# Optimization experiments

Hardware: AMD Instinct MI355X
Metric: run time of the kernel (lower is better)

The kernel has to match this reference:

```python
import jax, jax.numpy as jnp
import numpy as np

B, C, H, W = 4, 256, 64, 64
CQ = C // 8  # query/key projection dim


def setup_inputs() -> dict:
    key = jax.random.key(0)
    ks = jax.random.split(key, 8)
    s = 0.02
    return {
        "x": jax.random.normal(ks[0], (B, C, H, W), dtype=jnp.float32),
        "Wq": jax.random.normal(ks[1], (CQ, C), dtype=jnp.float32) * s,
        "bq": jnp.zeros((CQ,), dtype=jnp.float32),
        "Wk": jax.random.normal(ks[2], (CQ, C), dtype=jnp.float32) * s,
        "bk": jnp.zeros((CQ,), dtype=jnp.float32),
        "Wv": jax.random.normal(ks[3], (C, C), dtype=jnp.float32) * s,
        "bv": jnp.zeros((C,), dtype=jnp.float32),
        "gamma": jnp.zeros((1,), dtype=jnp.float32),
    }


def reference(x, Wq, bq, Wk, bk, Wv, bv, gamma):
    b, c, h, w = x.shape
    n = h * w
    xf = x.reshape(b, c, n)  # (B, C, N)
    # 1x1 convs == channel-wise linear maps
    q = jnp.einsum('oc,bcn->bon', Wq, xf) + bq[None, :, None]  # (B, C/8, N)
    k = jnp.einsum('oc,bcn->bon', Wk, xf) + bk[None, :, None]  # (B, C/8, N)
    v = jnp.einsum('oc,bcn->bon', Wv, xf) + bv[None, :, None]  # (B, C, N)
    # energy[b, n, m] = q[b, :, n] . k[b, :, m], scaled by sqrt(C)
    energy = jnp.einsum('bon,bom->bnm', q, k) / jnp.sqrt(jnp.asarray(c, x.dtype))
    attn = jax.nn.softmax(energy, axis=-1)  # softmax over keys m
    # out[b, c, m] = sum_n v[b, c, n] * attn[b, m, n]  (torch bmm(value, attn^T))
    out = jnp.einsum('bcn,bmn->bcm', v, attn)
    out = out.reshape(b, c, h, w)
    return gamma[0] * out + x
```

## Files before the change

kernel.cpp:

```cpp
#include <hip/hip_runtime.h>
#include <stdint.h>

#define B_ 4
#define C_ 256
#define N_ 4096
#define LOG2E 1.44269504088896341f
#define EXP2(x) __builtin_amdgcn_exp2f(x)

typedef __attribute__((ext_vector_type(8))) short short8;
typedef __attribute__((ext_vector_type(4))) float f32x4;

__device__ __forceinline__ unsigned short f2bf(float f) {
    unsigned int u = __float_as_uint(f);
    u += 0x7FFFu + ((u >> 16) & 1u);
    return (unsigned short)(u >> 16);
}

__device__ __forceinline__ unsigned int pack_bf(float a, float b) {
    unsigned int ua = __float_as_uint(a) + 0x8000u;
    unsigned int ub = __float_as_uint(b) + 0x8000u;
    return __builtin_amdgcn_perm(ub, ua, 0x07060302u);
}
__device__ __forceinline__ float bf_lo(unsigned int u) { return __uint_as_float(u << 16); }
__device__ __forceinline__ float bf_hi(unsigned int u) { return __uint_as_float(u & 0xFFFF0000u); }

__global__ __launch_bounds__(64) void prep_kernel(
    const float* __restrict__ Wq, const float* __restrict__ bq,
    const float* __restrict__ Wk, const float* __restrict__ bk,
    const float* __restrict__ Wv, const float* __restrict__ bv,
    unsigned short* __restrict__ wb, float* __restrict__ bb)
{
    const int m = blockIdx.x;
    const int t = threadIdx.x;
    const float* src;
    float scale = 1.0f, bias;
    if (m < 32)      { src = Wq + m * C_;        scale = 0.0625f * LOG2E; bias = bq[m] * 0.0625f * LOG2E; }
    else if (m < 64) { src = Wk + (m - 32) * C_;                          bias = bk[m - 32]; }
    else             { src = Wv + (m - 64) * C_;                          bias = bv[m - 64]; }
    float4 v = *(const float4*)(src + t * 4);
    unsigned int lo = (unsigned int)f2bf(v.x * scale) | ((unsigned int)f2bf(v.y * scale) << 16);
    unsigned int hi = (unsigned int)f2bf(v.z * scale) | ((unsigned int)f2bf(v.w * scale) << 16);
    *(uint2*)(wb + m * C_ + t * 4) = make_uint2(lo, hi);
    if (t == 0) bb[m] = bias;
}

__global__ __launch_bounds__(256) void proj_kernel(
    const float* __restrict__ x,
    const unsigned short* __restrict__ wb, const float* __restrict__ bb,
    unsigned short* __restrict__ qT, unsigned short* __restrict__ kT,
    unsigned short* __restrict__ vfrag)
{
    __shared__ unsigned short xs[256][68];

    const int bid = ((blockIdx.x & 7) << 5) + (blockIdx.x >> 3);
    const int b = bid >> 6, n0 = (bid & 63) << 6;
    const int jt = n0 >> 6;
    const int tid = threadIdx.x, wid = tid >> 6, lane = tid & 63;
    const int l15 = lane & 15, l4 = lane >> 4;

#pragma unroll
    for (int it = 0; it < 16; ++it) {
        int idx = it * 256 + tid;
        int k = idx >> 4, n4 = (idx & 15) << 2;
        float4 v = *(const float4*)(x + ((size_t)(b * C_ + k)) * N_ + n0 + n4);
        unsigned int lo = (unsigned int)f2bf(v.x) | ((unsigned int)f2bf(v.y) << 16);
        unsigned int hi = (unsigned int)f2bf(v.z) | ((unsigned int)f2bf(v.w) << 16);
        *(uint2*)&xs[k][n4] = make_uint2(lo, hi);
    }
    __syncthreads();

    const int m0 = wid * 80;
    f32x4 acc[5][4];
#pragma unroll
    for (int mf = 0; mf < 5; ++mf)
#pragma unroll
        for (int nt = 0; nt < 4; ++nt)
            acc[mf][nt] = (f32x4){0.f, 0.f, 0.f, 0.f};

#pragma unroll
    for (int s = 0; s < 8; ++s) {
        short8 wf[5];
#pragma unroll
        for (int mf = 0; mf < 5; ++mf)
            wf[mf] = *(const short8*)(wb + (size_t)(m0 + 16 * mf + l15) * C_ + 32 * s + 8 * l4);
        short8 xf[4];
#pragma unroll
        for (int nt = 0; nt < 4; ++nt) {
#pragma unroll
            for (int e = 0; e < 8; ++e)
                xf[nt][e] = (short)xs[32 * s + 8 * l4 + e][16 * nt + l15];
        }
#pragma unroll
        for (int mf = 0; mf < 5; ++mf)
#pragma unroll
            for (int nt = 0; nt < 4; ++nt)
                acc[mf][nt] = __builtin_amdgcn_mfma_f32_16x16x32_bf16(wf[mf], xf[nt], acc[mf][nt], 0, 0, 0);
    }

    __syncthreads();

#pragma unroll
    for (int mf = 0; mf < 5; ++mf) {
        const int mbase = m0 + 16 * mf + 4 * l4;
        const float4 b4 = *(const float4*)(bb + mbase);
        const int region = (m0 + 16 * mf) >> 5;
#pragma unroll
        for (int nt = 0; nt < 4; ++nt) {
            const int n = n0 + 16 * nt + l15;
            float o0 = acc[mf][nt][0] + b4.x;
            float o1 = acc[mf][nt][1] + b4.y;
            float o2 = acc[mf][nt][2] + b4.z;
            float o3 = acc[mf][nt][3] + b4.w;
            if (region == 0) {
                *(uint2*)(qT + ((size_t)(b * N_ + n)) * 32 + mbase) =
                    make_uint2(pack_bf(o0, o1), pack_bf(o2, o3));
            } else if (region == 1) {
                *(uint2*)(kT + ((size_t)(b * N_ + n)) * 32 + (mbase - 32)) =
                    make_uint2(pack_bf(o0, o1), pack_bf(o2, o3));
            } else {
                const int c = mbase - 64;
                const int nl = 16 * nt + l15;
                xs[c + 0][nl] = f2bf(o0);
                xs[c + 1][nl] = f2bf(o1);
                xs[c + 2][nl] = f2bf(o2);
                xs[c + 3][nl] = f2bf(o3);
            }
        }
    }

    __syncthreads();

    unsigned short* vout = vfrag + (((size_t)(b * 64 + jt)) << 14);
#pragma unroll
    for (int i = 0; i < 8; ++i) {
        const int fid = i * 256 + tid;
        const int c15 = fid & 15, fl4 = (fid >> 4) & 3, kb = (fid >> 6) & 1, cblk = (fid >> 7) & 15;
        short8 v = *(const short8*)&xs[cblk * 16 + c15][kb * 32 + fl4 * 8];
        *(short8*)(vout + (size_t)fid * 8) = v;
    }
}

__global__ __launch_bounds__(512, 2) void attn_part_kernel(
    const unsigned short* __restrict__ qT, const unsigned short* __restrict__ kT,
    const unsigned short* __restrict__ vfrag,
    unsigned short* __restrict__ po, float* __restrict__ mlb)
{
    __shared__ unsigned short Pl[2][64][72];

    const int raw = blockIdx.x;
    const int bid = ((raw & 7) << 6) | (raw >> 3);
    const int b = bid >> 7;
    const int qt = (bid >> 1) & 63;
    const int s = bid & 1;
    const int i0 = qt << 6;
    const int j0 = s << 11;
    const int tid = threadIdx.x, wid = tid >> 6, lane = tid & 63;
    const int l15 = lane & 15, l4 = lane >> 4;
    const f32x4 zero = {0.f, 0.f, 0.f, 0.f};

    if (wid < 4) {
        const short8 qfrag = *(const short8*)(
            qT + ((size_t)(b * N_ + i0 + 16 * wid + l15)) * 32 + 8 * l4);
        const unsigned short* kbase = kT + ((size_t)(b * N_ + j0) + l15) * 32 + 8 * l4;

        short8 ka[4], kb_[4];
        _Pragma("unroll")
        for (int f = 0; f < 4; ++f)
            ka[f] = *(const short8*)(kbase + (size_t)(16 * f) * 32);

        float l = 0.f;

#define QK_BODY(T, KC, KN)                                                        \
  {                                                                               \
    if ((T) < 31) {                                                               \
      _Pragma("unroll")                                                           \
      for (int f = 0; f < 4; ++f)                                                 \
        KN[f] = *(const short8*)(kbase + (size_t)(((T) + 1) * 64 + 16 * f) * 32); \
    }                                                                             \
    f32x4 sv[4];                                                                  \
    _Pragma("unroll")                                                             \
    for (int f = 0; f < 4; ++f)                                                   \
      sv[f] = __builtin_amdgcn_mfma_f32_16x16x32_bf16(KC[f], qfrag, zero, 0, 0, 0);\
    float ps = 0.f;                                                               \
    _Pragma("unroll")                                                             \
    for (int f = 0; f < 4; ++f) {                                                 \
      _Pragma("unroll")                                                           \
      for (int r = 0; r < 4; ++r) { sv[f][r] = EXP2(sv[f][r]); ps += sv[f][r]; }  \
    }                                                                             \
    ps += __shfl_xor(ps, 16, 64);                                                 \
    ps += __shfl_xor(ps, 32, 64);                                                 \
    l += ps;                                                                      \
    unsigned short* prow = &Pl[(T) & 1][16 * wid + l15][4 * l4];                  \
    _Pragma("unroll")                                                             \
    for (int f = 0; f < 4; ++f)                                                   \
      *(uint2*)(prow + 16 * f) = make_uint2(pack_bf(sv[f][0], sv[f][1]),          \
                                            pack_bf(sv[f][2], sv[f][3]));         \
  }

        for (int u = 0; u < 16; ++u) {
            QK_BODY(2 * u, ka, kb_)
            __syncthreads();
            QK_BODY(2 * u + 1, kb_, ka)
            __syncthreads();
        }
        if (l4 == 0)
            mlb[(size_t)bid * 64 + 16 * wid + l15] = l;
        __syncthreads();
    } else {
        const int c0 = (wid - 4) << 6;
        const unsigned short* vfb_ = vfrag + (((size_t)(b * 64 + s * 32)) << 14)
                                   + ((size_t)(c0 >> 4) << 10) + l4 * 128 + l15 * 8;

        f32x4 acc[4][4];
        _Pragma("unroll")
        for (int qf = 0; qf < 4; ++qf) {
            _Pragma("unroll")
            for (int nb = 0; nb < 4; ++nb)
                acc[qf][nb] = (f32x4){0.f, 0.f, 0.f, 0.f};
        }

        short8 va_[4][2], vb2_[4][2];

#define PV_LOAD(DST, T)                                                           \
    {                                                                             \
      _Pragma("unroll")                                                           \
      for (int nb = 0; nb < 4; ++nb) {                                            \
        _Pragma("unroll")                                                         \
        for (int kb = 0; kb < 2; ++kb)                                            \
          DST[nb][kb] = *(const short8*)(vfb_ + ((size_t)(T) << 14) + nb * 1024 + kb * 512); \
      }                                                                           \
    }

#define PV_BODY(T, VC, VN)                                                        \
  {                                                                               \
    if ((T) >= 1 && (T) < 32) PV_LOAD(VN, (T))                                    \
    const int bf = ((T) + 1) & 1;                                 \
    short8 pa[4][2];                                                              \
    _Pragma("unroll")                                                             \
    for (int qf = 0; qf < 4; ++qf) {                                              \
      _Pragma("unroll")                                                           \
      for (int kb = 0; kb < 2; ++kb)                                              \
        pa[qf][kb] = *(const short8*)&Pl[bf][16 * qf + l15][kb * 32 + 8 * l4];    \
    }                                                                             \
    __builtin_amdgcn_s_setprio(1);                                                \
    _Pragma("unroll")                                                             \
    for (int qf = 0; qf < 4; ++qf) {                                              \
      _Pragma("unroll")                                                           \
      for (int kb = 0; kb < 2; ++kb) {                                            \
        _Pragma("unroll")                                                         \
        for (int nb = 0; nb < 4; ++nb)                                            \
          acc[qf][nb] = __builtin_amdgcn_mfma_f32_16x16x32_bf16(pa[qf][kb], VC[nb][kb], acc[qf][nb], 0, 0, 0); \
      }                                                                           \
    }                                                                             \
    __builtin_amdgcn_s_setprio(0);                                                \
  }

        PV_LOAD(vb2_, 0)
        __syncthreads();
        for (int u = 0; u < 16; ++u) {
            PV_BODY(2 * u + 1, vb2_, va_)
            __syncthreads();
            PV_BODY(2 * u + 2, va_, vb2_)
            __syncthreads();
        }

        unsigned short* pbase = po + ((size_t)bid << 14);
        _Pragma("unroll")
        for (int qf = 0; qf < 4; ++qf) {
            _Pragma("unroll")
            for (int nb = 0; nb < 4; ++nb) {
                const int c = c0 + 16 * nb + l15;
                *(uint2*)(pbase + c * 64 + 16 * qf + 4 * l4) =
                    make_uint2(pack_bf(acc[qf][nb][0], acc[qf][nb][1]),
                               pack_bf(acc[qf][nb][2], acc[qf][nb][3]));
            }
        }
    }
}

__global__ __launch_bounds__(256) void reduce_kernel(
    const unsigned short* __restrict__ po, const float* __restrict__ mlb,
    const float* __restrict__ x, const float* __restrict__ gamma,
    float* __restrict__ out)
{
    __shared__ float al[64];

    const int bq = blockIdx.x >> 2;
    const int cq = blockIdx.x & 3;
    const int b = bq >> 6, qt = bq & 63;
    const int lid0 = bq << 1, lid1 = lid0 | 1;
    const int tid = threadIdx.x;

    if (tid < 64) {
        const float l0 = mlb[(size_t)lid0 * 64 + tid];
        const float l1 = mlb[(size_t)lid1 * 64 + tid];
        al[tid] = gamma[0] / (l0 + l1);
    }
    __syncthreads();

    const int i4 = tid & 15, c16 = tid >> 4;
    const float4 av = *(const float4*)&al[i4 * 4];

#pragma unroll
    for (int cc = 0; cc < 4; ++cc) {
        const int c = (cq << 6) + cc * 16 + c16;
        const uint2 p0 = *(const uint2*)(po + ((size_t)lid0 << 14) + c * 64 + i4 * 4);
        const uint2 p1 = *(const uint2*)(po + ((size_t)lid1 << 14) + c * 64 + i4 * 4);
        const size_t xi = ((size_t)(b * C_ + c)) * N_ + (qt << 6) + i4 * 4;
        const float4 xr = *(const float4*)(x + xi);
        float4 res;
        res.x = (bf_lo(p0.x) + bf_lo(p1.x)) * av.x + xr.x;
        res.y = (bf_hi(p0.x) + bf_hi(p1.x)) * av.y + xr.y;
        res.z = (bf_lo(p0.y) + bf_lo(p1.y)) * av.z + xr.z;
        res.w = (bf_hi(p0.y) + bf_hi(p1.y)) * av.w + xr.w;
        *(float4*)(out + xi) = res;
    }
}

extern "C" void kernel_launch(void* const* d_in, const int* in_sizes, int n_in,
                              void* d_out, int out_size, void* d_ws, size_t ws_size,
                              hipStream_t stream) {
    (void)in_sizes; (void)n_in; (void)out_size; (void)ws_size;
    const float* x  = (const float*)d_in[0];
    const float* Wq = (const float*)d_in[1];
    const float* bq = (const float*)d_in[2];
    const float* Wk = (const float*)d_in[3];
    const float* bk = (const float*)d_in[4];
    const float* Wv = (const float*)d_in[5];
    const float* bv = (const float*)d_in[6];
    const float* gm = (const float*)d_in[7];
    float* out = (float*)d_out;

    char* ws = (char*)d_ws;
    unsigned short* wb = (unsigned short*)ws;
    float*          bb = (float*)(ws + 320 * 256 * 2);
    unsigned short* qT = (unsigned short*)(ws + 320 * 256 * 2 + 320 * 4);
    unsigned short* kT = qT + (size_t)B_ * N_ * 32;
    unsigned short* vf = kT + (size_t)B_ * N_ * 32;
    unsigned short* po = vf + (size_t)B_ * C_ * N_;
    float*         mlb = (float*)(po + (size_t)512 * 16384);

    hipLaunchKernelGGL(prep_kernel, dim3(320), dim3(64), 0, stream,
                       Wq, bq, Wk, bk, Wv, bv, wb, bb);
    hipLaunchKernelGGL(proj_kernel, dim3(256), dim3(256), 0, stream,
                       x, wb, bb, qT, kT, vf);
    hipLaunchKernelGGL(attn_part_kernel, dim3(512), dim3(512), 0, stream,
                       qT, kT, vf, po, mlb);
    hipLaunchKernelGGL(reduce_kernel, dim3(1024), dim3(256), 0, stream,
                       po, mlb, x, gm, out);
}
```

Measured before the change: 78.22 us.

## Double query tile per attention block to reuse K and V loads

Each attention block now handles 128 query rows instead of 64. Each QK wave computes two 16-row fragments against the same K tiles, and each PV wave accumulates eight query fragments against the same V fragments. This halves global K/V traffic per query and halves the block count to 256, though each block now has more accumulator registers and LDS, and fewer blocks may leave compute units underfilled. The reduce kernel and workspace indexing are updated to match the 128-row tiles.

New measurement: 71.32 us. 8.8% less time.

```diff
diff --git a/kernel.cpp b/kernel.cpp
--- a/kernel.cpp
+++ b/kernel.cpp
@@ -145,22 +145,25 @@
     const unsigned short* __restrict__ vfrag,
     unsigned short* __restrict__ po, float* __restrict__ mlb)
 {
-    __shared__ unsigned short Pl[2][64][72];
+    __shared__ unsigned short Pl[2][128][72];
 
     const int raw = blockIdx.x;
-    const int bid = ((raw & 7) << 6) | (raw >> 3);
-    const int b = bid >> 7;
-    const int qt = (bid >> 1) & 63;
+    const int bid = ((raw & 7) << 5) | (raw >> 3);
+    const int b = bid >> 6;
+    const int qt = (bid >> 1) & 31;
     const int s = bid & 1;
-    const int i0 = qt << 6;
+    const int i0 = qt << 7;
     const int j0 = s << 11;
     const int tid = threadIdx.x, wid = tid >> 6, lane = tid & 63;
     const int l15 = lane & 15, l4 = lane >> 4;
     const f32x4 zero = {0.f, 0.f, 0.f, 0.f};
 
     if (wid < 4) {
-        const short8 qfrag = *(const short8*)(
-            qT + ((size_t)(b * N_ + i0 + 16 * wid + l15)) * 32 + 8 * l4);
+        const int r0 = i0 + 32 * wid;
+        const short8 qfrag0 = *(const short8*)(
+            qT + ((size_t)(b * N_ + r0 + l15)) * 32 + 8 * l4);
+        const short8 qfrag1 = *(const short8*)(
+            qT + ((size_t)(b * N_ + r0 + 16 + l15)) * 32 + 8 * l4);
         const unsigned short* kbase = kT + ((size_t)(b * N_ + j0) + l15) * 32 + 8 * l4;
 
         short8 ka[4], kb_[4];
@@ -168,7 +171,7 @@
         for (int f = 0; f < 4; ++f)
             ka[f] = *(const short8*)(kbase + (size_t)(16 * f) * 32);
 
-        float l = 0.f;
+        float l0 = 0.f, l1 = 0.f;
 
 #define QK_BODY(T, KC, KN)                                                        \
   {                                                                               \
@@ -177,24 +180,33 @@
       for (int f = 0; f < 4; ++f)                                                 \
         KN[f] = *(const short8*)(kbase + (size_t)(((T) + 1) * 64 + 16 * f) * 32); \
     }                                                                             \
-    f32x4 sv[4];                                                                  \
-    _Pragma("unroll")                                                             \
-    for (int f = 0; f < 4; ++f)                                                   \
-      sv[f] = __builtin_amdgcn_mfma_f32_16x16x32_bf16(KC[f], qfrag, zero, 0, 0, 0);\
-    float ps = 0.f;                                                               \
+    f32x4 sv0[4], sv1[4];                                                         \
     _Pragma("unroll")                                                             \
     for (int f = 0; f < 4; ++f) {                                                 \
-      _Pragma("unroll")                                                           \
-      for (int r = 0; r < 4; ++r) { sv[f][r] = EXP2(sv[f][r]); ps += sv[f][r]; }  \
-    }                                                                             \
-    ps += __shfl_xor(ps, 16, 64);                                                 \
-    ps += __shfl_xor(ps, 32, 64);                                                 \
-    l += ps;                                                                      \
-    unsigned short* prow = &Pl[(T) & 1][16 * wid + l15][4 * l4];                  \
+      sv0[f] = __builtin_amdgcn_mfma_f32_16x16x32_bf16(KC[f], qfrag0, zero, 0, 0, 0);\
+      sv1[f] = __builtin_amdgcn_mfma_f32_16x16x32_bf16(KC[f], qfrag1, zero, 0, 0, 0);\
+    }                                                                             \
+    float ps0 = 0.f, ps1 = 0.f;                                                   \
     _Pragma("unroll")                                                             \
-    for (int f = 0; f < 4; ++f)                                                   \
-      *(uint2*)(prow + 16 * f) = make_uint2(pack_bf(sv[f][0], sv[f][1]),          \
-                                            pack_bf(sv[f][2], sv[f][3]));         \
+    for (int f = 0; f < 4; ++f) {                                                 \
+      _Pragma("unroll")                                                           \
+      for (int r = 0; r < 4; ++r) {                                               \
+        sv0[f][r] = EXP2(sv0[f][r]); ps0 += sv0[f][r];                            \
+        sv1[f][r] = EXP2(sv1[f][r]); ps1 += sv1[f][r];                            \
+      }                                                                           \
+    }                                                                             \
+    ps0 += __shfl_xor(ps0, 16, 64);  ps1 += __shfl_xor(ps1, 16, 64);              \
+    ps0 += __shfl_xor(ps0, 32, 64);  ps1 += __shfl_xor(ps1, 32, 64);              \
+    l0 += ps0;  l1 += ps1;                                                        \
+    unsigned short* prow0 = &Pl[(T) & 1][32 * wid + l15][4 * l4];                 \
+    unsigned short* prow1 = &Pl[(T) & 1][32 * wid + 16 + l15][4 * l4];            \
+    _Pragma("unroll")                                                             \
+    for (int f = 0; f < 4; ++f) {                                                 \
+      *(uint2*)(prow0 + 16 * f) = make_uint2(pack_bf(sv0[f][0], sv0[f][1]),       \
+                                             pack_bf(sv0[f][2], sv0[f][3]));      \
+      *(uint2*)(prow1 + 16 * f) = make_uint2(pack_bf(sv1[f][0], sv1[f][1]),       \
+                                             pack_bf(sv1[f][2], sv1[f][3]));      \
+    }                                                                             \
   }
 
         for (int u = 0; u < 16; ++u) {
@@ -203,17 +215,19 @@
             QK_BODY(2 * u + 1, kb_, ka)
             __syncthreads();
         }
-        if (l4 == 0)
-            mlb[(size_t)bid * 64 + 16 * wid + l15] = l;
+        if (l4 == 0) {
+            mlb[(size_t)bid * 128 + 32 * wid + l15] = l0;
+            mlb[(size_t)bid * 128 + 32 * wid + 16 + l15] = l1;
+        }
         __syncthreads();
     } else {
         const int c0 = (wid - 4) << 6;
         const unsigned short* vfb_ = vfrag + (((size_t)(b * 64 + s * 32)) << 14)
                                    + ((size_t)(c0 >> 4) << 10) + l4 * 128 + l15 * 8;
 
-        f32x4 acc[4][4];
+        f32x4 acc[8][4];
         _Pragma("unroll")
-        for (int qf = 0; qf < 4; ++qf) {
+        for (int qf = 0; qf < 8; ++qf) {
             _Pragma("unroll")
             for (int nb = 0; nb < 4; ++nb)
                 acc[qf][nb] = (f32x4){0.f, 0.f, 0.f, 0.f};
@@ -235,22 +249,17 @@
   {                                                                               \
     if ((T) >= 1 && (T) < 32) PV_LOAD(VN, (T))                                    \
     const int bf = ((T) + 1) & 1;                                 \
-    short8 pa[4][2];                                                              \
-    _Pragma("unroll")                                                             \
-    for (int qf = 0; qf < 4; ++qf) {                                              \
-      _Pragma("unroll")                                                           \
-      for (int kb = 0; kb < 2; ++kb)                                              \
-        pa[qf][kb] = *(const short8*)&Pl[bf][16 * qf + l15][kb * 32 + 8 * l4];    \
-    }                                                                             \
     __builtin_amdgcn_s_setprio(1);                                                \
     _Pragma("unroll")                                                             \
-    for (int qf = 0; qf < 4; ++qf) {                                              \
-      _Pragma("unroll")                                                           \
-      for (int kb = 0; kb < 2; ++kb) {                                            \
-        _Pragma("unroll")                                                         \
-        for (int nb = 0; nb < 4; ++nb)                                            \
-          acc[qf][nb] = __builtin_amdgcn_mfma_f32_16x16x32_bf16(pa[qf][kb], VC[nb][kb], acc[qf][nb], 0, 0, 0); \
-      }                                                                           \
+    for (int qf = 0; qf < 8; ++qf) {                                              \
+      short8 pa0 = *(const short8*)&Pl[bf][16 * qf + l15][8 * l4];                \
+      short8 pa1 = *(const short8*)&Pl[bf][16 * qf + l15][32 + 8 * l4];           \
+      _Pragma("unroll")                                                           \
+      for (int nb = 0; nb < 4; ++nb)                                              \
+        acc[qf][nb] = __builtin_amdgcn_mfma_f32_16x16x32_bf16(pa0, VC[nb][0], acc[qf][nb], 0, 0, 0); \
+      _Pragma("unroll")                                                           \
+      for (int nb = 0; nb < 4; ++nb)                                              \
+        acc[qf][nb] = __builtin_amdgcn_mfma_f32_16x16x32_bf16(pa1, VC[nb][1], acc[qf][nb], 0, 0, 0); \
     }                                                                             \
     __builtin_amdgcn_s_setprio(0);                                                \
   }
@@ -264,13 +273,13 @@
             __syncthreads();
         }
 
-        unsigned short* pbase = po + ((size_t)bid << 14);
+        unsigned short* pbase = po + ((size_t)bid << 15);
         _Pragma("unroll")
-        for (int qf = 0; qf < 4; ++qf) {
+        for (int qf = 0; qf < 8; ++qf) {
             _Pragma("unroll")
             for (int nb = 0; nb < 4; ++nb) {
                 const int c = c0 + 16 * nb + l15;
-                *(uint2*)(pbase + c * 64 + 16 * qf + 4 * l4) =
+                *(uint2*)(pbase + c * 128 + 16 * qf + 4 * l4) =
                     make_uint2(pack_bf(acc[qf][nb][0], acc[qf][nb][1]),
                                pack_bf(acc[qf][nb][2], acc[qf][nb][3]));
             }
@@ -283,30 +292,30 @@
     const float* __restrict__ x, const float* __restrict__ gamma,
     float* __restrict__ out)
 {
-    __shared__ float al[64];
-
-    const int bq = blockIdx.x >> 2;
-    const int cq = blockIdx.x & 3;
-    const int b = bq >> 6, qt = bq & 63;
+    __shared__ float al[128];
+
+    const int bq = blockIdx.x >> 3;
+    const int cq = blockIdx.x & 7;
+    const int b = bq >> 5, qt = bq & 31;
     const int lid0 = bq << 1, lid1 = lid0 | 1;
     const int tid = threadIdx.x;
 
-    if (tid < 64) {
-        const float l0 = mlb[(size_t)lid0 * 64 + tid];
-        const float l1 = mlb[(size_t)lid1 * 64 + tid];
-        al[tid] = gamma[0] / (l0 + l1);
+    if (tid < 128) {
+        const float la = mlb[(size_t)lid0 * 128 + tid];
+        const float lb = mlb[(size_t)lid1 * 128 + tid];
+        al[tid] = gamma[0] / (la + lb);
     }
     __syncthreads();
 
-    const int i4 = tid & 15, c16 = tid >> 4;
+    const int i4 = tid & 31, ch = tid >> 5;
     const float4 av = *(const float4*)&al[i4 * 4];
 
 #pragma unroll
     for (int cc = 0; cc < 4; ++cc) {
-        const int c = (cq << 6) + cc * 16 + c16;
-        const uint2 p0 = *(const uint2*)(po + ((size_t)lid0 << 14) + c * 64 + i4 * 4);
-        const uint2 p1 = *(const uint2*)(po + ((size_t)lid1 << 14) + c * 64 + i4 * 4);
-        const size_t xi = ((size_t)(b * C_ + c)) * N_ + (qt << 6) + i4 * 4;
+        const int c = (cq << 5) + cc * 8 + ch;
+        const uint2 p0 = *(const uint2*)(po + ((size_t)lid0 << 15) + c * 128 + i4 * 4);
+        const uint2 p1 = *(const uint2*)(po + ((size_t)lid1 << 15) + c * 128 + i4 * 4);
+        const size_t xi = ((size_t)(b * C_ + c)) * N_ + (qt << 7) + i4 * 4;
         const float4 xr = *(const float4*)(x + xi);
         float4 res;
         res.x = (bf_lo(p0.x) + bf_lo(p1.x)) * av.x + xr.x;
@@ -338,13 +347,13 @@
     unsigned short* kT = qT + (size_t)B_ * N_ * 32;
     unsigned short* vf = kT + (size_t)B_ * N_ * 32;
     unsigned short* po = vf + (size_t)B_ * C_ * N_;
-    float*         mlb = (float*)(po + (size_t)512 * 16384);
+    float*         mlb = (float*)(po + (size_t)256 * 32768);
 
     hipLaunchKernelGGL(prep_kernel, dim3(320), dim3(64), 0, stream,
                        Wq, bq, Wk, bk, Wv, bv, wb, bb);
     hipLaunchKernelGGL(proj_kernel, dim3(256), dim3(256), 0, stream,
                        x, wb, bb, qT, kT, vf);
-    hipLaunchKernelGGL(attn_part_kernel, dim3(512), dim3(512), 0, stream,
+    hipLaunchKernelGGL(attn_part_kernel, dim3(256), dim3(512), 0, stream,
                        qT, kT, vf, po, mlb);
     hipLaunchKernelGGL(reduce_kernel, dim3(1024), dim3(256), 0, stream,
                        po, mlb, x, gm, out);
```
